# Performance work log

Hardware: AMD Instinct MI355X
Metric: run time of the kernel (lower is better)

## Reference

```python
import jax, jax.numpy as jnp
import numpy as np

N = 100000   # nodes
E = 1000000  # edges (before self-loops)
D_IN = 16
H, C = 2, 64  # heads, hidden per head
EPS = 1e-5    # BatchNorm eps
SLOPE = 0.2   # LeakyReLU negative slope (GATConv default)


def setup_inputs() -> dict:
    key = jax.random.key(0)
    ks = jax.random.split(key, 40)
    rn = lambda k, s, sc=0.1: jax.random.normal(k, s, jnp.float32) * sc
    inp = {}
    inp["x"] = jax.random.normal(ks[0], (N, D_IN), jnp.float32)
    inp["edge_index"] = jax.random.randint(ks[1], (2, E), 0, N)
    i = 2
    for l, din in ((1, D_IN), (2, C), (3, C)):
        inp[f"W{l}"] = rn(ks[i], (din, H * C)); i += 1
        inp[f"as{l}"] = rn(ks[i], (H, C)); i += 1
        inp[f"ad{l}"] = rn(ks[i], (H, C)); i += 1
        inp[f"b{l}"] = jnp.zeros((C,), jnp.float32)
        inp[f"g{l}"] = jnp.ones((C,), jnp.float32)   # BN gamma
        inp[f"be{l}"] = jnp.zeros((C,), jnp.float32) # BN beta
    inp["mW1"] = rn(ks[i], (C + 5, C)); i += 1
    inp["mb1"] = jnp.zeros((C,), jnp.float32)
    inp["mW2"] = rn(ks[i], (C, C)); i += 1
    inp["mb2"] = jnp.zeros((C,), jnp.float32)
    inp["pW"] = rn(ks[i], (C, 1)); i += 1
    inp["pb"] = jnp.zeros((1,), jnp.float32)
    inp["vW"] = rn(ks[i], (C, 1)); i += 1
    inp["vb"] = jnp.zeros((1,), jnp.float32)
    return inp


def gat(x, src, dst, W, att_s, att_d, bias):
    # GATConv, heads=H, concat=False (mean over heads). Messages flow src->dst.
    h = (x @ W).reshape(-1, H, C)               # [N,H,C]
    a_s = jnp.sum(h * att_s, -1)                # [N,H]
    a_d = jnp.sum(h * att_d, -1)                # [N,H]
    e = jax.nn.leaky_relu(a_s[src] + a_d[dst], SLOPE)  # [Etot,H]
    e = e - jax.ops.segment_max(e, dst, num_segments=N)[dst]
    ee = jnp.exp(e)
    alpha = ee / (jax.ops.segment_sum(ee, dst, num_segments=N)[dst] + 1e-16)
    msg = h[src] * alpha[:, :, None]            # [Etot,H,C]
    out = jax.ops.segment_sum(msg, dst, num_segments=N)  # [N,H,C]
    return out.mean(1) + bias                   # [N,C]


def bn(h, g, b):
    m = h.mean(0)
    v = jnp.mean((h - m) ** 2, 0)  # biased variance (torch BN normalization)
    return (h - m) * jax.lax.rsqrt(v + EPS) * g + b


def reference(x, edge_index, W1, as1, ad1, b1, g1, be1,
              W2, as2, ad2, b2, g2, be2, W3, as3, ad3, b3, g3, be3,
              mW1, mb1, mW2, mb2, pW, pb, vW, vb):
    loops = jnp.arange(N)
    src = jnp.concatenate([edge_index[0], loops])  # add_self_loops=True
    dst = jnp.concatenate([edge_index[1], loops])
    ctx = x[:, 9:14]  # context features [N,5]
    h = jax.nn.relu(bn(gat(x, src, dst, W1, as1, ad1, b1), g1, be1))
    h = jax.nn.relu(bn(gat(h, src, dst, W2, as2, ad2, b2), g2, be2))
    h = jax.nn.relu(bn(gat(h, src, dst, W3, as3, ad3, b3), g3, be3))
    # dropout is identity in eval reference
    h = jnp.concatenate([h, ctx], axis=1)          # [N, C+5]
    h = jax.nn.relu(h @ mW1 + mb1) @ mW2 + mb2     # MLP
    logits = (h @ pW + pb).squeeze(-1)             # [N]
    value = (h @ vW + vb).squeeze(-1)              # [N]
    return logits, value
```

## Files before the change

### kernel.cpp

```cpp
#include <hip/hip_runtime.h>
#include <hip/hip_fp16.h>


__device__ __forceinline__ float leaky(float x) { return x > 0.f ? x : 0.2f * x; }

#define BCAP 4096
#define NSL 256

__global__ void bucket_hist(const int* __restrict__ dst, int* __restrict__ bcnt, int E) {
  __shared__ int cnt[512];
  int t = threadIdx.x;
  cnt[t] = 0; cnt[t + 256] = 0;
  __syncthreads();
  for (int e = blockIdx.x * blockDim.x + t; e < E; e += gridDim.x * blockDim.x)
    atomicAdd(&cnt[dst[e] >> 8], 1);
  __syncthreads();
  for (int i = t; i < 512; i += 256)
    if (cnt[i]) atomicAdd(&bcnt[i], cnt[i]);
}

__global__ void bucket_scan(const int* __restrict__ bcnt, int* __restrict__ boff,
                            int* __restrict__ bcur, int nbk) {
  __shared__ int temp[512];
  int t = threadIdx.x;
  int v = (t < nbk) ? bcnt[t] : 0;
  temp[t] = v;
  __syncthreads();
  for (int off = 1; off < 512; off <<= 1) {
    int add = (t >= off) ? temp[t - off] : 0;
    __syncthreads();
    temp[t] += add;
    __syncthreads();
  }
  if (t < nbk) {
    int ex = temp[t] - v;
    boff[t] = ex;
    bcur[t] = ex;
  }
}

__global__ __launch_bounds__(256) void bin_scatter(
    const int* __restrict__ src, const int* __restrict__ dst,
    int* __restrict__ bcur, int2* __restrict__ ebuf, int E) {
  __shared__ int cnt[512];
  __shared__ int base[512];
  int t = threadIdx.x;
  int beg = blockIdx.x * 8192;
  int end = min(E, beg + 8192);
  cnt[t] = 0; cnt[t + 256] = 0;
  __syncthreads();
  for (int e = beg + t; e < end; e += 256)
    atomicAdd(&cnt[dst[e] >> 8], 1);
  __syncthreads();
  for (int i = t; i < 512; i += 256) {
    base[i] = cnt[i] ? atomicAdd(&bcur[i], cnt[i]) : 0;
    cnt[i] = 0;
  }
  __syncthreads();
  for (int e = beg + t; e < end; e += 256) {
    int d = dst[e];
    int bk = d >> 8;
    int off = atomicAdd(&cnt[bk], 1);
    ebuf[base[bk] + off] = make_int2(src[e], d);
  }
}

__global__ __launch_bounds__(256) void bucket_sort(
    const int2* __restrict__ ebuf, const int* __restrict__ boff,
    int2* __restrict__ col2, int* __restrict__ row_ptr, int E, int n, int nbk) {
  __shared__ int2 eds[BCAP];
  __shared__ int dcnt[256];
  __shared__ int dbase[256];
  __shared__ int dexcl[256];
  int b = blockIdx.x, t = threadIdx.x;
  int S = boff[b];
  int Eend = (b + 1 < nbk) ? boff[b + 1] : E;
  int cnt = min(Eend - S, BCAP);
  for (int i = t; i < cnt; i += 256) eds[i] = ebuf[S + i];
  dcnt[t] = 0;
  __syncthreads();
  for (int i = t; i < cnt; i += 256) atomicAdd(&dcnt[eds[i].y & 255], 1);
  __syncthreads();
  int v = dcnt[t];
  dbase[t] = v;
  __syncthreads();
  for (int off = 1; off < 256; off <<= 1) {
    int add = (t >= off) ? dbase[t - off] : 0;
    __syncthreads();
    dbase[t] += add;
    __syncthreads();
  }
  int excl = dbase[t] - v;
  int d = (b << 8) + t;
  if (d < n) row_ptr[d] = S + excl;
  if (b == nbk - 1 && t == 0) row_ptr[n] = E;
  dcnt[t] = 0;
  dexcl[t] = excl;
  __syncthreads();
  for (int i = t; i < cnt; i += 256) {
    int2 e = eds[i];
    int dl = e.y & 255;
    int off = atomicAdd(&dcnt[dl], 1);
    col2[S + dexcl[dl] + off] = e;
  }
}

__global__ __launch_bounds__(256) void bn_stats(const float* __restrict__ h,
                                                float* __restrict__ stats, int n) {
  __shared__ float ssum[64], ssq[64];
  int t = threadIdx.x;
  if (t < 64) { ssum[t] = 0.f; ssq[t] = 0.f; }
  __syncthreads();
  const float4* h4 = (const float4*)h;
  size_t total4 = (size_t)n * 16;
  size_t stride = (size_t)gridDim.x * blockDim.x;
  int cbase = ((int)(((size_t)blockIdx.x * blockDim.x + t) & 15)) * 4;
  float s0 = 0.f, s1 = 0.f, s2 = 0.f, s3 = 0.f;
  float q0 = 0.f, q1 = 0.f, q2 = 0.f, q3 = 0.f;
  for (size_t i = (size_t)blockIdx.x * blockDim.x + t; i < total4; i += stride) {
    float4 v = h4[i];
    s0 += v.x; q0 = fmaf(v.x, v.x, q0);
    s1 += v.y; q1 = fmaf(v.y, v.y, q1);
    s2 += v.z; q2 = fmaf(v.z, v.z, q2);
    s3 += v.w; q3 = fmaf(v.w, v.w, q3);
  }
  atomicAdd(&ssum[cbase + 0], s0); atomicAdd(&ssq[cbase + 0], q0);
  atomicAdd(&ssum[cbase + 1], s1); atomicAdd(&ssq[cbase + 1], q1);
  atomicAdd(&ssum[cbase + 2], s2); atomicAdd(&ssq[cbase + 2], q2);
  atomicAdd(&ssum[cbase + 3], s3); atomicAdd(&ssq[cbase + 3], q3);
  __syncthreads();
  if (t < 64) {
    stats[blockIdx.x * 128 + t] = ssum[t];
    stats[blockIdx.x * 128 + 64 + t] = ssq[t];
  }
}

__global__ void bn_finalize(const float* __restrict__ stats, const float* __restrict__ g,
                            const float* __restrict__ be, float* __restrict__ scsh,
                            float inv_n) {
  __shared__ float red[128];
  int t = threadIdx.x;
  int c = t & 63;
  int off = (t >> 6) * 64;
  float acc = 0.f;
  for (int b = 0; b < NSL; b++) acc += stats[b * 128 + off + c];
  red[t] = acc;
  __syncthreads();
  if (t < 64) {
    float mean = red[t] * inv_n;
    float var = red[64 + t] * inv_n - mean * mean;
    float sc = rsqrtf(var + 1e-5f) * g[t];
    scsh[t] = sc;
    scsh[64 + t] = be[t] - mean * sc;
  }
}

template <int K, bool BN>
__global__ __launch_bounds__(256) void gat_project_tiled(
    const float* __restrict__ act, const float* __restrict__ scsh,
    const float* __restrict__ W,
    const float* __restrict__ att_s, const float* __restrict__ att_d,
    __half2* __restrict__ hb, float* __restrict__ as_,
    float* __restrict__ ad_, int n) {
  constexpr int AST = K + 4;
  __shared__ float aS[64 * AST];
  __shared__ float wS[K * 128];
  __shared__ float attS[256];

  int t = threadIdx.x;
  int node0 = blockIdx.x * 64;
  int rows = min(64, n - node0);

  constexpr int AF4 = 64 * K / 4;
  for (int i = t; i < AF4; i += 256) {
    int r = i / (K / 4), kc = i % (K / 4);
    float4 v = make_float4(0.f, 0.f, 0.f, 0.f);
    if (r < rows) v = *(const float4*)&act[(size_t)(node0 + r) * K + kc * 4];
    if (BN) {
      float4 sc4 = *(const float4*)&scsh[kc * 4];
      float4 sh4 = *(const float4*)&scsh[64 + kc * 4];
      v.x = fmaxf(fmaf(v.x, sc4.x, sh4.x), 0.f);
      v.y = fmaxf(fmaf(v.y, sc4.y, sh4.y), 0.f);
      v.z = fmaxf(fmaf(v.z, sc4.z, sh4.z), 0.f);
      v.w = fmaxf(fmaf(v.w, sc4.w, sh4.w), 0.f);
    }
    *(float4*)&aS[r * AST + kc * 4] = v;
  }
  constexpr int WF4 = K * 32;
  for (int i = t; i < WF4; i += 256)
    *(float4*)&wS[i * 4] = *(const float4*)&W[i * 4];
  attS[t] = (t < 128) ? att_s[t] : att_d[t - 128];
  __syncthreads();

  int tc = t & 15, tr = t >> 4;
  int c0 = tc * 8, r0 = tr * 4;

  float acc[4][8] = {};
  for (int k = 0; k < K; k += 4) {
    float4 av[4];
    float4 wv[4][2];
#pragma unroll
    for (int i = 0; i < 4; i++) av[i] = *(const float4*)&aS[(r0 + i) * AST + k];
#pragma unroll
    for (int kk = 0; kk < 4; kk++) {
      wv[kk][0] = *(const float4*)&wS[(k + kk) * 128 + c0];
      wv[kk][1] = *(const float4*)&wS[(k + kk) * 128 + c0 + 4];
    }
#pragma unroll
    for (int i = 0; i < 4; i++) {
      const float* ai = (const float*)&av[i];
#pragma unroll
      for (int kk = 0; kk < 4; kk++) {
        const float* w0 = (const float*)&wv[kk][0];
        const float* w1 = (const float*)&wv[kk][1];
#pragma unroll
        for (int j = 0; j < 4; j++) {
          acc[i][j] = fmaf(ai[kk], w0[j], acc[i][j]);
          acc[i][4 + j] = fmaf(ai[kk], w1[j], acc[i][4 + j]);
        }
      }
    }
  }

#pragma unroll
  for (int i = 0; i < 4; i++) {
    int r = r0 + i;
    float psv = 0.f, pdv = 0.f;
#pragma unroll
    for (int j = 0; j < 8; j++) {
      psv = fmaf(acc[i][j], attS[c0 + j], psv);
      pdv = fmaf(acc[i][j], attS[128 + c0 + j], pdv);
    }
    psv += __shfl_xor(psv, 1); pdv += __shfl_xor(pdv, 1);
    psv += __shfl_xor(psv, 2); pdv += __shfl_xor(pdv, 2);
    psv += __shfl_xor(psv, 4); pdv += __shfl_xor(pdv, 4);
    if (r < rows) {
      size_t base = (size_t)(node0 + r) * 64 + (c0 >> 1);
      hb[base + 0] = __floats2half2_rn(acc[i][0], acc[i][1]);
      hb[base + 1] = __floats2half2_rn(acc[i][2], acc[i][3]);
      hb[base + 2] = __floats2half2_rn(acc[i][4], acc[i][5]);
      hb[base + 3] = __floats2half2_rn(acc[i][6], acc[i][7]);
      if (tc == 0 || tc == 8) {
        int head = tc >> 3;
        as_[(node0 + r) * 2 + head] = psv;
        ad_[(node0 + r) * 2 + head] = pdv;
      }
    }
  }
}

__device__ __forceinline__ void fma8(float* a, float my, uint4 raw) {
  float2 f;
  f = __half22float2(__builtin_bit_cast(__half2, raw.x)); a[0] = fmaf(my, f.x, a[0]); a[1] = fmaf(my, f.y, a[1]);
  f = __half22float2(__builtin_bit_cast(__half2, raw.y)); a[2] = fmaf(my, f.x, a[2]); a[3] = fmaf(my, f.y, a[3]);
  f = __half22float2(__builtin_bit_cast(__half2, raw.z)); a[4] = fmaf(my, f.x, a[4]); a[5] = fmaf(my, f.y, a[5]);
  f = __half22float2(__builtin_bit_cast(__half2, raw.w)); a[6] = fmaf(my, f.x, a[6]); a[7] = fmaf(my, f.y, a[7]);
}

__global__ __launch_bounds__(256) void gat_aggregate(
    const __half2* __restrict__ hb,
    const float* __restrict__ as_, const float* __restrict__ ad_,
    const int* __restrict__ row_ptr, const int2* __restrict__ col2,
    const float* __restrict__ bias, float* __restrict__ out, int n) {
  int wave = (int)((blockIdx.x * blockDim.x + threadIdx.x) >> 6);
  int lane = threadIdx.x & 63;
  if (wave >= n) return;
  int d = wave;
  int sub = lane >> 4, q = lane & 15;
  bool head1 = (q >= 8);
  int hidx = head1 ? 1 : 0;
  int beg = row_ptr[d], end = row_ptr[d + 1];
  const uint4* hb4 = (const uint4*)hb;

  float2 dv = *(const float2*)&ad_[d * 2];
  float ad_my = head1 ? dv.y : dv.x;

  float a[8] = {};
  float dpart = 0.f;

  if (sub == 0) {
    float asv = as_[d * 2 + hidx];
    float my = __expf(leaky(asv + ad_my));
    uint4 raw = hb4[(size_t)d * 16 + q];
    fma8(a, my, raw);
    dpart = my;
  }

  int k = beg;
  for (; k + 7 < end; k += 8) {
    int kkA = k + sub, kkB = k + 4 + sub;
    int sA = col2[kkA].x;
    int sB = col2[kkB].x;
    float asA = as_[sA * 2 + hidx];
    float asB = as_[sB * 2 + hidx];
    uint4 rawA = hb4[(size_t)sA * 16 + q];
    uint4 rawB = hb4[(size_t)sB * 16 + q];
    float myA = __expf(leaky(asA + ad_my));
    float myB = __expf(leaky(asB + ad_my));
    fma8(a, myA, rawA);
    dpart += myA;
    fma8(a, myB, rawB);
    dpart += myB;
  }
  if (k + 3 < end) {
    int kk = k + sub;
    int s = col2[kk].x;
    float asv = as_[s * 2 + hidx];
    uint4 raw = hb4[(size_t)s * 16 + q];
    float my = __expf(leaky(asv + ad_my));
    fma8(a, my, raw);
    dpart += my;
    k += 4;
  }
  int rem = end - k;
  if (sub < rem) {
    int kk = k + sub;
    int s = col2[kk].x;
    float asv = as_[s * 2 + hidx];
    uint4 raw = hb4[(size_t)s * 16 + q];
    float my = __expf(leaky(asv + ad_my));
    fma8(a, my, raw);
    dpart += my;
  }

#pragma unroll
  for (int i = 0; i < 8; i++) a[i] += __shfl(a[i], lane ^ 16);
  dpart += __shfl(dpart, lane ^ 16);
#pragma unroll
  for (int i = 0; i < 8; i++) a[i] += __shfl(a[i], lane ^ 32);
  float dsum = dpart + __shfl(dpart, lane ^ 32);

  int src = (lane + 8) & 63;
  float b[8];
#pragma unroll
  for (int i = 0; i < 8; i++) b[i] = __shfl(a[i], src);
  float den1 = __shfl(dsum, src);
  if (lane < 8) {
    float r0 = 1.f / (dsum + 1e-16f), r1 = 1.f / (den1 + 1e-16f);
    float4 bl = *(const float4*)&bias[q * 8];
    float4 bh = *(const float4*)&bias[q * 8 + 4];
    float4 o0, o1;
    o0.x = 0.5f * (a[0] * r0 + b[0] * r1) + bl.x;
    o0.y = 0.5f * (a[1] * r0 + b[1] * r1) + bl.y;
    o0.z = 0.5f * (a[2] * r0 + b[2] * r1) + bl.z;
    o0.w = 0.5f * (a[3] * r0 + b[3] * r1) + bl.w;
    o1.x = 0.5f * (a[4] * r0 + b[4] * r1) + bh.x;
    o1.y = 0.5f * (a[5] * r0 + b[5] * r1) + bh.y;
    o1.z = 0.5f * (a[6] * r0 + b[6] * r1) + bh.z;
    o1.w = 0.5f * (a[7] * r0 + b[7] * r1) + bh.w;
    *(float4*)&out[(size_t)d * 64 + q * 8] = o0;
    *(float4*)&out[(size_t)d * 64 + q * 8 + 4] = o1;
  }
}

__global__ __launch_bounds__(256) void mlp_head_tiled(
    const float* __restrict__ h3raw, const float* __restrict__ scsh,
    const float* __restrict__ x,
    const float* __restrict__ mW1, const float* __restrict__ mb1,
    const float* __restrict__ mW2, const float* __restrict__ mb2,
    const float* __restrict__ pW, const float* __restrict__ pb,
    const float* __restrict__ vW, const float* __restrict__ vb,
    float* __restrict__ out, int n) {
  __shared__ float lds[13632];
  float* a1  = lds;
  float* ctx = lds + 4352;
  float* a2  = lds + 4864;
  float* w1  = lds + 9216;
  float* w2  = lds;

  int t = threadIdx.x;
  int node0 = blockIdx.x * 64;
  int rows = min(64, n - node0);

#pragma unroll
  for (int i = 0; i < 4; i++) {
    int flat = t + i * 256;
    int r = flat >> 4, kc = flat & 15;
    float4 v = make_float4(0.f, 0.f, 0.f, 0.f);
    if (r < rows) v = *(const float4*)&h3raw[(size_t)(node0 + r) * 64 + kc * 4];
    float4 sc4 = *(const float4*)&scsh[kc * 4];
    float4 sh4 = *(const float4*)&scsh[64 + kc * 4];
    v.x = fmaxf(fmaf(v.x, sc4.x, sh4.x), 0.f);
    v.y = fmaxf(fmaf(v.y, sc4.y, sh4.y), 0.f);
    v.z = fmaxf(fmaf(v.z, sc4.z, sh4.z), 0.f);
    v.w = fmaxf(fmaf(v.w, sc4.w, sh4.w), 0.f);
    *(float4*)&a1[r * 68 + kc * 4] = v;
  }
  for (int i = t; i < 320; i += 256) {
    int r = i / 5, j = i % 5;
    ctx[r * 8 + j] = (r < rows) ? x[(size_t)(node0 + r) * 16 + 9 + j] : 0.f;
  }
#pragma unroll
  for (int i = 0; i < 5; i++) {
    int flat = t + i * 256;
    if (flat < 1104) *(float4*)&w1[flat * 4] = *(const float4*)&mW1[flat * 4];
  }
  __syncthreads();

  int tc = t & 15, tr = t >> 4;
  int c0 = tc * 4, r0 = tr * 4;

  float acc[4][4] = {};
  for (int k = 0; k < 64; k += 4) {
    float4 av[4], wv[4];
#pragma unroll
    for (int i = 0; i < 4; i++) av[i] = *(const float4*)&a1[(r0 + i) * 68 + k];
#pragma unroll
    for (int j = 0; j < 4; j++) wv[j] = *(const float4*)&w1[(k + j) * 64 + c0];
#pragma unroll
    for (int i = 0; i < 4; i++) {
      const float* ai = (const float*)&av[i];
#pragma unroll
      for (int kk = 0; kk < 4; kk++) {
        const float* wr = (const float*)&wv[kk];
        acc[i][0] = fmaf(ai[kk], wr[0], acc[i][0]);
        acc[i][1] = fmaf(ai[kk], wr[1], acc[i][1]);
        acc[i][2] = fmaf(ai[kk], wr[2], acc[i][2]);
        acc[i][3] = fmaf(ai[kk], wr[3], acc[i][3]);
      }
    }
  }
#pragma unroll
  for (int k = 64; k < 69; k++) {
    float4 wv = *(const float4*)&w1[k * 64 + c0];
    const float* wr = (const float*)&wv;
#pragma unroll
    for (int i = 0; i < 4; i++) {
      float a = ctx[(r0 + i) * 8 + (k - 64)];
      acc[i][0] = fmaf(a, wr[0], acc[i][0]);
      acc[i][1] = fmaf(a, wr[1], acc[i][1]);
      acc[i][2] = fmaf(a, wr[2], acc[i][2]);
      acc[i][3] = fmaf(a, wr[3], acc[i][3]);
    }
  }
  float b1v0 = mb1[c0], b1v1 = mb1[c0 + 1], b1v2 = mb1[c0 + 2], b1v3 = mb1[c0 + 3];
#pragma unroll
  for (int i = 0; i < 4; i++) {
    float4 t1;
    t1.x = fmaxf(acc[i][0] + b1v0, 0.f);
    t1.y = fmaxf(acc[i][1] + b1v1, 0.f);
    t1.z = fmaxf(acc[i][2] + b1v2, 0.f);
    t1.w = fmaxf(acc[i][3] + b1v3, 0.f);
    *(float4*)&a2[(r0 + i) * 68 + c0] = t1;
  }
  __syncthreads();

#pragma unroll
  for (int i = 0; i < 4; i++) {
    int flat = t + i * 256;
    *(float4*)&w2[flat * 4] = *(const float4*)&mW2[flat * 4];
  }
  __syncthreads();

  float acc2[4][4] = {};
  for (int k = 0; k < 64; k += 4) {
    float4 av[4], wv[4];
#pragma unroll
    for (int i = 0; i < 4; i++) av[i] = *(const float4*)&a2[(r0 + i) * 68 + k];
#pragma unroll
    for (int j = 0; j < 4; j++) wv[j] = *(const float4*)&w2[(k + j) * 64 + c0];
#pragma unroll
    for (int i = 0; i < 4; i++) {
      const float* ai = (const float*)&av[i];
#pragma unroll
      for (int kk = 0; kk < 4; kk++) {
        const float* wr = (const float*)&wv[kk];
        acc2[i][0] = fmaf(ai[kk], wr[0], acc2[i][0]);
        acc2[i][1] = fmaf(ai[kk], wr[1], acc2[i][1]);
        acc2[i][2] = fmaf(ai[kk], wr[2], acc2[i][2]);
        acc2[i][3] = fmaf(ai[kk], wr[3], acc2[i][3]);
      }
    }
  }

  float b2v[4], pwv[4], vwv[4];
#pragma unroll
  for (int j = 0; j < 4; j++) {
    b2v[j] = mb2[c0 + j];
    pwv[j] = pW[c0 + j];
    vwv[j] = vW[c0 + j];
  }
  float p[4], v[4];
#pragma unroll
  for (int i = 0; i < 4; i++) {
    float ps = 0.f, vs = 0.f;
#pragma unroll
    for (int j = 0; j < 4; j++) {
      float u = acc2[i][j] + b2v[j];
      ps = fmaf(u, pwv[j], ps);
      vs = fmaf(u, vwv[j], vs);
    }
    p[i] = ps; v[i] = vs;
  }
#pragma unroll
  for (int off = 1; off < 16; off <<= 1) {
#pragma unroll
    for (int i = 0; i < 4; i++) {
      p[i] += __shfl_xor(p[i], off);
      v[i] += __shfl_xor(v[i], off);
    }
  }
  if (tc == 0) {
    float pbs = pb[0], vbs = vb[0];
#pragma unroll
    for (int i = 0; i < 4; i++) {
      int r = r0 + i;
      if (r < rows) {
        out[node0 + r] = p[i] + pbs;
        out[n + node0 + r] = v[i] + vbs;
      }
    }
  }
}

extern "C" void kernel_launch(void* const* d_in, const int* in_sizes, int n_in,
                              void* d_out, int out_size, void* d_ws, size_t ws_size,
                              hipStream_t stream) {
  const float* x = (const float*)d_in[0];
  const int* ei = (const int*)d_in[1];
  const float* W[3]  = {(const float*)d_in[2],  (const float*)d_in[8],  (const float*)d_in[14]};
  const float* AS[3] = {(const float*)d_in[3],  (const float*)d_in[9],  (const float*)d_in[15]};
  const float* AD[3] = {(const float*)d_in[4],  (const float*)d_in[10], (const float*)d_in[16]};
  const float* B[3]  = {(const float*)d_in[5],  (const float*)d_in[11], (const float*)d_in[17]};
  const float* G[3]  = {(const float*)d_in[6],  (const float*)d_in[12], (const float*)d_in[18]};
  const float* BE[3] = {(const float*)d_in[7],  (const float*)d_in[13], (const float*)d_in[19]};
  const float* mW1 = (const float*)d_in[20];
  const float* mb1 = (const float*)d_in[21];
  const float* mW2 = (const float*)d_in[22];
  const float* mb2 = (const float*)d_in[23];
  const float* pW  = (const float*)d_in[24];
  const float* pb  = (const float*)d_in[25];
  const float* vW  = (const float*)d_in[26];
  const float* vb  = (const float*)d_in[27];

  const int N = in_sizes[0] / 16;
  const int E = in_sizes[1] / 2;
  const int* srcp = ei;
  const int* dstp = ei + E;

  float* bufB  = (float*)d_ws;
  float* hbuf  = bufB + (size_t)N * 64;
  float* as_   = hbuf + (size_t)N * 64;
  float* ad_   = as_ + (size_t)N * 2;
  float* stats = ad_ + (size_t)N * 2;
  float* scsh  = stats + NSL * 128;
  int* row_ptr = (int*)(scsh + 128);
  int* bcnt    = row_ptr + (N + 1);
  int* boff    = bcnt + 512;
  int* bcur    = boff + 512;
  int2* col2   = (int2*)(bcur + 512);
  int2* ebuf   = col2 + E;
  __half2* hb  = (__half2*)hbuf;

  const int nbk = (N + 255) >> 8;
  const float inv_n = 1.0f / (float)N;

  hipMemsetAsync(bcnt, 0, sizeof(int) * 512, stream);
  bucket_hist<<<256, 256, 0, stream>>>(dstp, bcnt, E);
  bucket_scan<<<1, 512, 0, stream>>>(bcnt, boff, bcur, nbk);
  bin_scatter<<<(E + 8191) / 8192, 256, 0, stream>>>(srcp, dstp, bcur, ebuf, E);
  bucket_sort<<<nbk, 256, 0, stream>>>(ebuf, boff, col2, row_ptr, E, N, nbk);

  const int tiles = (N + 63) / 64;

  for (int l = 0; l < 3; l++) {
    if (l == 0)
      gat_project_tiled<16, false><<<tiles, 256, 0, stream>>>(x, scsh, W[l], AS[l], AD[l],
                                                              hb, as_, ad_, N);
    else
      gat_project_tiled<64, true><<<tiles, 256, 0, stream>>>(bufB, scsh, W[l], AS[l], AD[l],
                                                             hb, as_, ad_, N);
    gat_aggregate<<<(N + 3) / 4, 256, 0, stream>>>(hb, as_, ad_, row_ptr, col2,
                                                   B[l], bufB, N);
    bn_stats<<<NSL, 256, 0, stream>>>(bufB, stats, N);
    bn_finalize<<<1, 128, 0, stream>>>(stats, G[l], BE[l], scsh, inv_n);
  }

  mlp_head_tiled<<<tiles, 256, 0, stream>>>(bufB, scsh, x, mW1, mb1, mW2, mb2,
                                            pW, pb, vW, vb, (float*)d_out, N);
}
```

Before: 505.7 us.

## Fuse BatchNorm statistics into GAT aggregation and restructure edge gather

Removes the separate bn_stats pass by having gat_aggregate accumulate per-channel sums and squared sums in LDS and atomically add them into sliced global stats buffers, which bn_finalize reads and then zeroes for the next layer. The aggregation loop is also reworked so that each lane computes the attention exponentials for one edge of a 64-edge chunk (including the self loop as an extra item), then broadcasts source index and weights via shuffles while quads of lanes gather feature rows. This avoids re-reading the 100k×64 output for BN, but adds shared and global atomics per node and more shuffle traffic in the inner loop.

Measured after the change: 660.2 us. 30.6% more time.

```diff
diff --git a/kernel.cpp b/kernel.cpp
--- a/kernel.cpp
+++ b/kernel.cpp
@@ -105,37 +105,7 @@
   }
 }
 
-__global__ __launch_bounds__(256) void bn_stats(const float* __restrict__ h,
-                                                float* __restrict__ stats, int n) {
-  __shared__ float ssum[64], ssq[64];
-  int t = threadIdx.x;
-  if (t < 64) { ssum[t] = 0.f; ssq[t] = 0.f; }
-  __syncthreads();
-  const float4* h4 = (const float4*)h;
-  size_t total4 = (size_t)n * 16;
-  size_t stride = (size_t)gridDim.x * blockDim.x;
-  int cbase = ((int)(((size_t)blockIdx.x * blockDim.x + t) & 15)) * 4;
-  float s0 = 0.f, s1 = 0.f, s2 = 0.f, s3 = 0.f;
-  float q0 = 0.f, q1 = 0.f, q2 = 0.f, q3 = 0.f;
-  for (size_t i = (size_t)blockIdx.x * blockDim.x + t; i < total4; i += stride) {
-    float4 v = h4[i];
-    s0 += v.x; q0 = fmaf(v.x, v.x, q0);
-    s1 += v.y; q1 = fmaf(v.y, v.y, q1);
-    s2 += v.z; q2 = fmaf(v.z, v.z, q2);
-    s3 += v.w; q3 = fmaf(v.w, v.w, q3);
-  }
-  atomicAdd(&ssum[cbase + 0], s0); atomicAdd(&ssq[cbase + 0], q0);
-  atomicAdd(&ssum[cbase + 1], s1); atomicAdd(&ssq[cbase + 1], q1);
-  atomicAdd(&ssum[cbase + 2], s2); atomicAdd(&ssq[cbase + 2], q2);
-  atomicAdd(&ssum[cbase + 3], s3); atomicAdd(&ssq[cbase + 3], q3);
-  __syncthreads();
-  if (t < 64) {
-    stats[blockIdx.x * 128 + t] = ssum[t];
-    stats[blockIdx.x * 128 + 64 + t] = ssq[t];
-  }
-}
-
-__global__ void bn_finalize(const float* __restrict__ stats, const float* __restrict__ g,
+__global__ void bn_finalize(float* __restrict__ stats, const float* __restrict__ g,
                             const float* __restrict__ be, float* __restrict__ scsh,
                             float inv_n) {
   __shared__ float red[128];
@@ -143,7 +113,11 @@
   int c = t & 63;
   int off = (t >> 6) * 64;
   float acc = 0.f;
-  for (int b = 0; b < NSL; b++) acc += stats[b * 128 + off + c];
+  for (int b = 0; b < NSL; b++) {
+    int i = b * 128 + off + c;
+    acc += stats[i];
+    stats[i] = 0.f;
+  }
   red[t] = acc;
   __syncthreads();
   if (t < 64) {
@@ -261,95 +235,108 @@
     const __half2* __restrict__ hb,
     const float* __restrict__ as_, const float* __restrict__ ad_,
     const int* __restrict__ row_ptr, const int2* __restrict__ col2,
-    const float* __restrict__ bias, float* __restrict__ out, int n) {
-  int wave = (int)((blockIdx.x * blockDim.x + threadIdx.x) >> 6);
-  int lane = threadIdx.x & 63;
-  if (wave >= n) return;
-  int d = wave;
+    const float* __restrict__ bias, float* __restrict__ out,
+    float* __restrict__ stats, int n) {
+  __shared__ float ssum[64], ssq[64];
+  int t = threadIdx.x;
+  if (t < 64) { ssum[t] = 0.f; ssq[t] = 0.f; }
+  __syncthreads();
+
+  int d = (int)((blockIdx.x * blockDim.x + t) >> 6);
+  int lane = t & 63;
+  bool active = d < n;
+  int dd = active ? d : 0;
+
   int sub = lane >> 4, q = lane & 15;
-  bool head1 = (q >= 8);
-  int hidx = head1 ? 1 : 0;
-  int beg = row_ptr[d], end = row_ptr[d + 1];
-  const uint4* hb4 = (const uint4*)hb;
-
-  float2 dv = *(const float2*)&ad_[d * 2];
-  float ad_my = head1 ? dv.y : dv.x;
+  bool head1 = q >= 8;
 
   float a[8] = {};
-  float dpart = 0.f;
-
-  if (sub == 0) {
-    float asv = as_[d * 2 + hidx];
-    float my = __expf(leaky(asv + ad_my));
-    uint4 raw = hb4[(size_t)d * 16 + q];
-    fma8(a, my, raw);
-    dpart = my;
-  }
-
-  int k = beg;
-  for (; k + 7 < end; k += 8) {
-    int kkA = k + sub, kkB = k + 4 + sub;
-    int sA = col2[kkA].x;
-    int sB = col2[kkB].x;
-    float asA = as_[sA * 2 + hidx];
-    float asB = as_[sB * 2 + hidx];
-    uint4 rawA = hb4[(size_t)sA * 16 + q];
-    uint4 rawB = hb4[(size_t)sB * 16 + q];
-    float myA = __expf(leaky(asA + ad_my));
-    float myB = __expf(leaky(asB + ad_my));
-    fma8(a, myA, rawA);
-    dpart += myA;
-    fma8(a, myB, rawB);
-    dpart += myB;
-  }
-  if (k + 3 < end) {
-    int kk = k + sub;
-    int s = col2[kk].x;
-    float asv = as_[s * 2 + hidx];
-    uint4 raw = hb4[(size_t)s * 16 + q];
-    float my = __expf(leaky(asv + ad_my));
-    fma8(a, my, raw);
-    dpart += my;
-    k += 4;
-  }
-  int rem = end - k;
-  if (sub < rem) {
-    int kk = k + sub;
-    int s = col2[kk].x;
-    float asv = as_[s * 2 + hidx];
-    uint4 raw = hb4[(size_t)s * 16 + q];
-    float my = __expf(leaky(asv + ad_my));
-    fma8(a, my, raw);
-    dpart += my;
+  float den0 = 0.f, den1 = 0.f;
+
+  if (active) {
+    int beg = row_ptr[dd];
+    int end = row_ptr[dd + 1];
+    int deg = end - beg;
+    int nItems = deg + 1;
+    float2 adv = *(const float2*)((const char*)ad_ + ((uint32_t)dd << 3));
+    const char* hbp = (const char*)hb;
+
+    for (int cbase = 0; cbase < nItems; cbase += 64) {
+      int nc = min(64, nItems - cbase);
+      int item = cbase + lane;
+      int s = dd;
+      float e0 = 0.f, e1 = 0.f;
+      if (item < nItems) {
+        if (item < deg)
+          s = *(const int*)((const char*)col2 + ((uint32_t)(beg + item) << 3));
+        float2 asv = *(const float2*)((const char*)as_ + ((uint32_t)s << 3));
+        e0 = __expf(leaky(asv.x + adv.x));
+        e1 = __expf(leaky(asv.y + adv.y));
+        den0 += e0; den1 += e1;
+      }
+      int rounds = (nc + 3) >> 2;
+      for (int rr = 0; rr < rounds; rr += 4) {
+        int nr = min(4, rounds - rr);
+        uint4 raw[4];
+        float myv[4];
+#pragma unroll
+        for (int r = 0; r < 4; r++) {
+          if (r < nr) {
+            int idx = ((rr + r) << 2) + sub;
+            int se = __shfl(s, idx);
+            float m0 = __shfl(e0, idx);
+            float m1 = __shfl(e1, idx);
+            myv[r] = head1 ? m1 : m0;
+            raw[r] = *(const uint4*)(hbp + (((uint32_t)se << 8) + (q << 4)));
+          }
+        }
+#pragma unroll
+        for (int r = 0; r < 4; r++)
+          if (r < nr) fma8(a, myv[r], raw[r]);
+      }
+    }
   }
 
 #pragma unroll
   for (int i = 0; i < 8; i++) a[i] += __shfl(a[i], lane ^ 16);
-  dpart += __shfl(dpart, lane ^ 16);
 #pragma unroll
   for (int i = 0; i < 8; i++) a[i] += __shfl(a[i], lane ^ 32);
-  float dsum = dpart + __shfl(dpart, lane ^ 32);
-
-  int src = (lane + 8) & 63;
+#pragma unroll
+  for (int off = 1; off < 64; off <<= 1) {
+    den0 += __shfl_xor(den0, off);
+    den1 += __shfl_xor(den1, off);
+  }
+  int srcl = (lane + 8) & 63;
   float b[8];
 #pragma unroll
-  for (int i = 0; i < 8; i++) b[i] = __shfl(a[i], src);
-  float den1 = __shfl(dsum, src);
-  if (lane < 8) {
-    float r0 = 1.f / (dsum + 1e-16f), r1 = 1.f / (den1 + 1e-16f);
+  for (int i = 0; i < 8; i++) b[i] = __shfl(a[i], srcl);
+
+  if (active && lane < 8) {
+    float r0 = 1.f / (den0 + 1e-16f), r1 = 1.f / (den1 + 1e-16f);
     float4 bl = *(const float4*)&bias[q * 8];
     float4 bh = *(const float4*)&bias[q * 8 + 4];
-    float4 o0, o1;
-    o0.x = 0.5f * (a[0] * r0 + b[0] * r1) + bl.x;
-    o0.y = 0.5f * (a[1] * r0 + b[1] * r1) + bl.y;
-    o0.z = 0.5f * (a[2] * r0 + b[2] * r1) + bl.z;
-    o0.w = 0.5f * (a[3] * r0 + b[3] * r1) + bl.w;
-    o1.x = 0.5f * (a[4] * r0 + b[4] * r1) + bh.x;
-    o1.y = 0.5f * (a[5] * r0 + b[5] * r1) + bh.y;
-    o1.z = 0.5f * (a[6] * r0 + b[6] * r1) + bh.z;
-    o1.w = 0.5f * (a[7] * r0 + b[7] * r1) + bh.w;
-    *(float4*)&out[(size_t)d * 64 + q * 8] = o0;
-    *(float4*)&out[(size_t)d * 64 + q * 8 + 4] = o1;
+    float o[8];
+    o[0] = 0.5f * (a[0] * r0 + b[0] * r1) + bl.x;
+    o[1] = 0.5f * (a[1] * r0 + b[1] * r1) + bl.y;
+    o[2] = 0.5f * (a[2] * r0 + b[2] * r1) + bl.z;
+    o[3] = 0.5f * (a[3] * r0 + b[3] * r1) + bl.w;
+    o[4] = 0.5f * (a[4] * r0 + b[4] * r1) + bh.x;
+    o[5] = 0.5f * (a[5] * r0 + b[5] * r1) + bh.y;
+    o[6] = 0.5f * (a[6] * r0 + b[6] * r1) + bh.z;
+    o[7] = 0.5f * (a[7] * r0 + b[7] * r1) + bh.w;
+    *(float4*)&out[(size_t)d * 64 + q * 8] = *(float4*)&o[0];
+    *(float4*)&out[(size_t)d * 64 + q * 8 + 4] = *(float4*)&o[4];
+#pragma unroll
+    for (int j = 0; j < 8; j++) {
+      atomicAdd(&ssum[q * 8 + j], o[j]);
+      atomicAdd(&ssq[q * 8 + j], o[j] * o[j]);
+    }
+  }
+  __syncthreads();
+  if (t < 64) {
+    int base = (int)(blockIdx.x & (NSL - 1)) * 128;
+    atomicAdd(&stats[base + t], ssum[t]);
+    atomicAdd(&stats[base + 64 + t], ssq[t]);
   }
 }
 
@@ -542,20 +529,20 @@
   float* hbuf  = bufB + (size_t)N * 64;
   float* as_   = hbuf + (size_t)N * 64;
   float* ad_   = as_ + (size_t)N * 2;
-  float* stats = ad_ + (size_t)N * 2;
-  float* scsh  = stats + NSL * 128;
+  float* scsh  = ad_ + (size_t)N * 2;
   int* row_ptr = (int*)(scsh + 128);
-  int* bcnt    = row_ptr + (N + 1);
-  int* boff    = bcnt + 512;
+  int* boff    = row_ptr + ((N + 2) & ~1);
   int* bcur    = boff + 512;
-  int2* col2   = (int2*)(bcur + 512);
+  int* bcnt    = bcur + 512;
+  float* stats = (float*)(bcnt + 512);
+  int2* col2   = (int2*)(stats + NSL * 128);
   int2* ebuf   = col2 + E;
   __half2* hb  = (__half2*)hbuf;
 
   const int nbk = (N + 255) >> 8;
   const float inv_n = 1.0f / (float)N;
 
-  hipMemsetAsync(bcnt, 0, sizeof(int) * 512, stream);
+  hipMemsetAsync(bcnt, 0, sizeof(int) * (512 + NSL * 128), stream);
   bucket_hist<<<256, 256, 0, stream>>>(dstp, bcnt, E);
   bucket_scan<<<1, 512, 0, stream>>>(bcnt, boff, bcur, nbk);
   bin_scatter<<<(E + 8191) / 8192, 256, 0, stream>>>(srcp, dstp, bcur, ebuf, E);
@@ -571,8 +558,7 @@
       gat_project_tiled<64, true><<<tiles, 256, 0, stream>>>(bufB, scsh, W[l], AS[l], AD[l],
                                                              hb, as_, ad_, N);
     gat_aggregate<<<(N + 3) / 4, 256, 0, stream>>>(hb, as_, ad_, row_ptr, col2,
-                                                   B[l], bufB, N);
-    bn_stats<<<NSL, 256, 0, stream>>>(bufB, stats, N);
+                                                   B[l], bufB, stats, N);
     bn_finalize<<<1, 128, 0, stream>>>(stats, G[l], BE[l], scsh, inv_n);
   }
 
```

## Fuse BatchNorm statistics into GAT aggregation epilogue and parallelize finalize

Applied to the files above, without the earlier changes.

The per-channel sum and sum-of-squares for BatchNorm are now accumulated in the aggregation kernel's epilogue through LDS atomics, then added into one of 256 global slots chosen by block index. This removes the separate bn_stats kernel and its full re-read of the N×64 output. bn_finalize now uses 1024 threads, zeroes the slots after reading them for the next layer, and the workspace is reordered so one memset clears both counters and stats. Output stores become nontemporal. The cost is extra LDS and global atomics in every aggregation block, plus a __syncthreads in a kernel that previously had none.

After: 643.0 us. 1.27x slower.

```diff
diff --git a/kernel.cpp b/kernel.cpp
--- a/kernel.cpp
+++ b/kernel.cpp
@@ -3,6 +3,8 @@
 
 
 __device__ __forceinline__ float leaky(float x) { return x > 0.f ? x : 0.2f * x; }
+
+typedef float f32x4 __attribute__((ext_vector_type(4)));
 
 #define BCAP 4096
 #define NSL 256
@@ -105,46 +107,27 @@
   }
 }
 
-__global__ __launch_bounds__(256) void bn_stats(const float* __restrict__ h,
-                                                float* __restrict__ stats, int n) {
-  __shared__ float ssum[64], ssq[64];
-  int t = threadIdx.x;
-  if (t < 64) { ssum[t] = 0.f; ssq[t] = 0.f; }
-  __syncthreads();
-  const float4* h4 = (const float4*)h;
-  size_t total4 = (size_t)n * 16;
-  size_t stride = (size_t)gridDim.x * blockDim.x;
-  int cbase = ((int)(((size_t)blockIdx.x * blockDim.x + t) & 15)) * 4;
-  float s0 = 0.f, s1 = 0.f, s2 = 0.f, s3 = 0.f;
-  float q0 = 0.f, q1 = 0.f, q2 = 0.f, q3 = 0.f;
-  for (size_t i = (size_t)blockIdx.x * blockDim.x + t; i < total4; i += stride) {
-    float4 v = h4[i];
-    s0 += v.x; q0 = fmaf(v.x, v.x, q0);
-    s1 += v.y; q1 = fmaf(v.y, v.y, q1);
-    s2 += v.z; q2 = fmaf(v.z, v.z, q2);
-    s3 += v.w; q3 = fmaf(v.w, v.w, q3);
-  }
-  atomicAdd(&ssum[cbase + 0], s0); atomicAdd(&ssq[cbase + 0], q0);
-  atomicAdd(&ssum[cbase + 1], s1); atomicAdd(&ssq[cbase + 1], q1);
-  atomicAdd(&ssum[cbase + 2], s2); atomicAdd(&ssq[cbase + 2], q2);
-  atomicAdd(&ssum[cbase + 3], s3); atomicAdd(&ssq[cbase + 3], q3);
-  __syncthreads();
-  if (t < 64) {
-    stats[blockIdx.x * 128 + t] = ssum[t];
-    stats[blockIdx.x * 128 + 64 + t] = ssq[t];
-  }
-}
-
-__global__ void bn_finalize(const float* __restrict__ stats, const float* __restrict__ g,
-                            const float* __restrict__ be, float* __restrict__ scsh,
-                            float inv_n) {
-  __shared__ float red[128];
-  int t = threadIdx.x;
-  int c = t & 63;
-  int off = (t >> 6) * 64;
+__global__ __launch_bounds__(1024) void bn_finalize(
+    float* __restrict__ stats, const float* __restrict__ g,
+    const float* __restrict__ be, float* __restrict__ scsh, float inv_n) {
+  __shared__ float red[1024];
+  int t = threadIdx.x;
+  int c = t & 127;
+  int grp = t >> 7;
   float acc = 0.f;
-  for (int b = 0; b < NSL; b++) acc += stats[b * 128 + off + c];
+  for (int b = grp; b < NSL; b += 8) {
+    int i = b * 128 + c;
+    acc += stats[i];
+    stats[i] = 0.f;
+  }
   red[t] = acc;
+  __syncthreads();
+  if (t < 128) {
+    float s = red[t];
+#pragma unroll
+    for (int j = 1; j < 8; j++) s += red[t + 128 * j];
+    red[t] = s;
+  }
   __syncthreads();
   if (t < 64) {
     float mean = red[t] * inv_n;
@@ -261,66 +244,74 @@
     const __half2* __restrict__ hb,
     const float* __restrict__ as_, const float* __restrict__ ad_,
     const int* __restrict__ row_ptr, const int2* __restrict__ col2,
-    const float* __restrict__ bias, float* __restrict__ out, int n) {
-  int wave = (int)((blockIdx.x * blockDim.x + threadIdx.x) >> 6);
-  int lane = threadIdx.x & 63;
-  if (wave >= n) return;
-  int d = wave;
+    const float* __restrict__ bias, float* __restrict__ out,
+    float* __restrict__ stats, int n) {
+  __shared__ float ssum[64], ssq[64];
+  int t = threadIdx.x;
+  if (t < 64) { ssum[t] = 0.f; ssq[t] = 0.f; }
+  __syncthreads();
+
+  int d = (int)((blockIdx.x * blockDim.x + t) >> 6);
+  int lane = t & 63;
+  bool active = d < n;
   int sub = lane >> 4, q = lane & 15;
   bool head1 = (q >= 8);
   int hidx = head1 ? 1 : 0;
-  int beg = row_ptr[d], end = row_ptr[d + 1];
-  const uint4* hb4 = (const uint4*)hb;
-
-  float2 dv = *(const float2*)&ad_[d * 2];
-  float ad_my = head1 ? dv.y : dv.x;
 
   float a[8] = {};
   float dpart = 0.f;
 
-  if (sub == 0) {
-    float asv = as_[d * 2 + hidx];
-    float my = __expf(leaky(asv + ad_my));
-    uint4 raw = hb4[(size_t)d * 16 + q];
-    fma8(a, my, raw);
-    dpart = my;
-  }
-
-  int k = beg;
-  for (; k + 7 < end; k += 8) {
-    int kkA = k + sub, kkB = k + 4 + sub;
-    int sA = col2[kkA].x;
-    int sB = col2[kkB].x;
-    float asA = as_[sA * 2 + hidx];
-    float asB = as_[sB * 2 + hidx];
-    uint4 rawA = hb4[(size_t)sA * 16 + q];
-    uint4 rawB = hb4[(size_t)sB * 16 + q];
-    float myA = __expf(leaky(asA + ad_my));
-    float myB = __expf(leaky(asB + ad_my));
-    fma8(a, myA, rawA);
-    dpart += myA;
-    fma8(a, myB, rawB);
-    dpart += myB;
-  }
-  if (k + 3 < end) {
-    int kk = k + sub;
-    int s = col2[kk].x;
-    float asv = as_[s * 2 + hidx];
-    uint4 raw = hb4[(size_t)s * 16 + q];
-    float my = __expf(leaky(asv + ad_my));
-    fma8(a, my, raw);
-    dpart += my;
-    k += 4;
-  }
-  int rem = end - k;
-  if (sub < rem) {
-    int kk = k + sub;
-    int s = col2[kk].x;
-    float asv = as_[s * 2 + hidx];
-    uint4 raw = hb4[(size_t)s * 16 + q];
-    float my = __expf(leaky(asv + ad_my));
-    fma8(a, my, raw);
-    dpart += my;
+  if (active) {
+    int beg = row_ptr[d], end = row_ptr[d + 1];
+    const uint4* hb4 = (const uint4*)hb;
+
+    float2 dv = *(const float2*)&ad_[d * 2];
+    float ad_my = head1 ? dv.y : dv.x;
+
+    if (sub == 0) {
+      float asv = as_[d * 2 + hidx];
+      float my = __expf(leaky(asv + ad_my));
+      uint4 raw = hb4[(size_t)d * 16 + q];
+      fma8(a, my, raw);
+      dpart = my;
+    }
+
+    int k = beg;
+    for (; k + 7 < end; k += 8) {
+      int kkA = k + sub, kkB = k + 4 + sub;
+      int sA = col2[kkA].x;
+      int sB = col2[kkB].x;
+      float asA = as_[sA * 2 + hidx];
+      float asB = as_[sB * 2 + hidx];
+      uint4 rawA = hb4[(size_t)sA * 16 + q];
+      uint4 rawB = hb4[(size_t)sB * 16 + q];
+      float myA = __expf(leaky(asA + ad_my));
+      float myB = __expf(leaky(asB + ad_my));
+      fma8(a, myA, rawA);
+      dpart += myA;
+      fma8(a, myB, rawB);
+      dpart += myB;
+    }
+    if (k + 3 < end) {
+      int kk = k + sub;
+      int s = col2[kk].x;
+      float asv = as_[s * 2 + hidx];
+      uint4 raw = hb4[(size_t)s * 16 + q];
+      float my = __expf(leaky(asv + ad_my));
+      fma8(a, my, raw);
+      dpart += my;
+      k += 4;
+    }
+    int rem = end - k;
+    if (sub < rem) {
+      int kk = k + sub;
+      int s = col2[kk].x;
+      float asv = as_[s * 2 + hidx];
+      uint4 raw = hb4[(size_t)s * 16 + q];
+      float my = __expf(leaky(asv + ad_my));
+      fma8(a, my, raw);
+      dpart += my;
+    }
   }
 
 #pragma unroll
@@ -330,26 +321,41 @@
   for (int i = 0; i < 8; i++) a[i] += __shfl(a[i], lane ^ 32);
   float dsum = dpart + __shfl(dpart, lane ^ 32);
 
-  int src = (lane + 8) & 63;
+  int srcl = (lane + 8) & 63;
   float b[8];
 #pragma unroll
-  for (int i = 0; i < 8; i++) b[i] = __shfl(a[i], src);
-  float den1 = __shfl(dsum, src);
-  if (lane < 8) {
+  for (int i = 0; i < 8; i++) b[i] = __shfl(a[i], srcl);
+  float den1 = __shfl(dsum, srcl);
+
+  if (active && lane < 8) {
     float r0 = 1.f / (dsum + 1e-16f), r1 = 1.f / (den1 + 1e-16f);
     float4 bl = *(const float4*)&bias[q * 8];
     float4 bh = *(const float4*)&bias[q * 8 + 4];
-    float4 o0, o1;
-    o0.x = 0.5f * (a[0] * r0 + b[0] * r1) + bl.x;
-    o0.y = 0.5f * (a[1] * r0 + b[1] * r1) + bl.y;
-    o0.z = 0.5f * (a[2] * r0 + b[2] * r1) + bl.z;
-    o0.w = 0.5f * (a[3] * r0 + b[3] * r1) + bl.w;
-    o1.x = 0.5f * (a[4] * r0 + b[4] * r1) + bh.x;
-    o1.y = 0.5f * (a[5] * r0 + b[5] * r1) + bh.y;
-    o1.z = 0.5f * (a[6] * r0 + b[6] * r1) + bh.z;
-    o1.w = 0.5f * (a[7] * r0 + b[7] * r1) + bh.w;
-    *(float4*)&out[(size_t)d * 64 + q * 8] = o0;
-    *(float4*)&out[(size_t)d * 64 + q * 8 + 4] = o1;
+    float o[8];
+    o[0] = 0.5f * (a[0] * r0 + b[0] * r1) + bl.x;
+    o[1] = 0.5f * (a[1] * r0 + b[1] * r1) + bl.y;
+    o[2] = 0.5f * (a[2] * r0 + b[2] * r1) + bl.z;
+    o[3] = 0.5f * (a[3] * r0 + b[3] * r1) + bl.w;
+    o[4] = 0.5f * (a[4] * r0 + b[4] * r1) + bh.x;
+    o[5] = 0.5f * (a[5] * r0 + b[5] * r1) + bh.y;
+    o[6] = 0.5f * (a[6] * r0 + b[6] * r1) + bh.z;
+    o[7] = 0.5f * (a[7] * r0 + b[7] * r1) + bh.w;
+    f32x4 o0 = {o[0], o[1], o[2], o[3]};
+    f32x4 o1 = {o[4], o[5], o[6], o[7]};
+    f32x4* outp = (f32x4*)&out[(size_t)d * 64 + q * 8];
+    __builtin_nontemporal_store(o0, outp);
+    __builtin_nontemporal_store(o1, outp + 1);
+#pragma unroll
+    for (int j = 0; j < 8; j++) {
+      atomicAdd(&ssum[q * 8 + j], o[j]);
+      atomicAdd(&ssq[q * 8 + j], o[j] * o[j]);
+    }
+  }
+  __syncthreads();
+  if (t < 64) {
+    int base = (int)(blockIdx.x & (NSL - 1)) * 128;
+    atomicAdd(&stats[base + t], ssum[t]);
+    atomicAdd(&stats[base + 64 + t], ssq[t]);
   }
 }
 
@@ -542,20 +548,20 @@
   float* hbuf  = bufB + (size_t)N * 64;
   float* as_   = hbuf + (size_t)N * 64;
   float* ad_   = as_ + (size_t)N * 2;
-  float* stats = ad_ + (size_t)N * 2;
-  float* scsh  = stats + NSL * 128;
+  float* scsh  = ad_ + (size_t)N * 2;
   int* row_ptr = (int*)(scsh + 128);
-  int* bcnt    = row_ptr + (N + 1);
-  int* boff    = bcnt + 512;
+  int* boff    = row_ptr + ((N + 2) & ~1);
   int* bcur    = boff + 512;
-  int2* col2   = (int2*)(bcur + 512);
+  int* bcnt    = bcur + 512;
+  float* stats = (float*)(bcnt + 512);
+  int2* col2   = (int2*)(stats + NSL * 128);
   int2* ebuf   = col2 + E;
   __half2* hb  = (__half2*)hbuf;
 
   const int nbk = (N + 255) >> 8;
   const float inv_n = 1.0f / (float)N;
 
-  hipMemsetAsync(bcnt, 0, sizeof(int) * 512, stream);
+  hipMemsetAsync(bcnt, 0, sizeof(int) * (512 + NSL * 128), stream);
   bucket_hist<<<256, 256, 0, stream>>>(dstp, bcnt, E);
   bucket_scan<<<1, 512, 0, stream>>>(bcnt, boff, bcur, nbk);
   bin_scatter<<<(E + 8191) / 8192, 256, 0, stream>>>(srcp, dstp, bcur, ebuf, E);
@@ -571,9 +577,8 @@
       gat_project_tiled<64, true><<<tiles, 256, 0, stream>>>(bufB, scsh, W[l], AS[l], AD[l],
                                                              hb, as_, ad_, N);
     gat_aggregate<<<(N + 3) / 4, 256, 0, stream>>>(hb, as_, ad_, row_ptr, col2,
-                                                   B[l], bufB, N);
-    bn_stats<<<NSL, 256, 0, stream>>>(bufB, stats, N);
-    bn_finalize<<<1, 128, 0, stream>>>(stats, G[l], BE[l], scsh, inv_n);
+                                                   B[l], bufB, stats, N);
+    bn_finalize<<<1, 1024, 0, stream>>>(stats, G[l], BE[l], scsh, inv_n);
   }
 
   mlp_head_tiled<<<tiles, 256, 0, stream>>>(bufB, scsh, x, mW1, mb1, mW2, mb2,
```
